# Performance work log

Hardware: AMD Instinct MI355X
Metric: run time of the kernel (lower is better)

The kernel has to match this reference:

```python
import jax, jax.numpy as jnp
import numpy as np

M, K, E = 4096, 7168, 2048  # tokens, hidden_size, expert_dim

def setup_inputs() -> dict:
    key = jax.random.key(0)
    k1, k2, k3 = jax.random.split(key, 3)
    x = jax.random.normal(k1, (M, K), dtype=jnp.float32)
    # NT layout: weights stored [n, k]
    w_up_gate = jax.random.normal(k2, (2 * E, K), dtype=jnp.float32) * (1.0 / np.sqrt(K))
    w_down = jax.random.normal(k3, (K, E), dtype=jnp.float32) * (1.0 / np.sqrt(E))
    return {"x": x, "w_up_gate": w_up_gate, "w_down": w_down}

def reference(x, w_up_gate, w_down):
    # up_gate GEMM: [m, k] @ [n, k]^T -> [m, 2*E]
    ug = jnp.einsum('mk,nk->mn', x, w_up_gate)
    gate, up = jnp.split(ug, 2, axis=-1)          # each [m, E]
    h = jax.nn.silu(gate) * up                     # SwiGLU activation
    # down GEMM: [m, E] @ [hidden, E]^T -> [m, hidden]
    out = jnp.einsum('me,he->mh', h, w_down)
    return out
```

## Files before the change

### kernel.cpp

```cpp
#include <hip/hip_runtime.h>
#include <hip/hip_bf16.h>
#include <stdint.h>

typedef __attribute__((ext_vector_type(8))) short     bf16x8;
typedef __attribute__((ext_vector_type(4))) float     f32x4;

__device__ __forceinline__ unsigned short f2bf(float f) {
  unsigned int u = __float_as_uint(f);
  u += 0x7FFFu + ((u >> 16) & 1u);
  return (unsigned short)(u >> 16);
}

__device__ __forceinline__ void async_cp16(const void* g, void* l) {
  __builtin_amdgcn_global_load_lds((const __attribute__((address_space(1))) void*)g,
                                   (__attribute__((address_space(3))) void*)l,
                                   16, 0, 0);
}

__global__ __launch_bounds__(256) void cvt_f32_to_bf16(const float* __restrict__ in,
                                                       unsigned short* __restrict__ out,
                                                       int n4) {
  int i = blockIdx.x * blockDim.x + threadIdx.x;
  const int stride = gridDim.x * blockDim.x;
  for (; i < n4; i += stride) {
    const float4 v = ((const float4*)in)[i];
    ushort4 o;
    o.x = f2bf(v.x); o.y = f2bf(v.y); o.z = f2bf(v.z); o.w = f2bf(v.w);
    ((ushort4*)out)[i] = o;
  }
}

__global__ __launch_bounds__(256) void cvt_wug_perm(const float* __restrict__ in,
                                                    unsigned short* __restrict__ out,
                                                    int n4) {
  int i = blockIdx.x * blockDim.x + threadIdx.x;
  const int stride = gridDim.x * blockDim.x;
  for (; i < n4; i += stride) {
    const int r = i / 1792, c = i - r * 1792;
    const int g = r >> 5, w = r & 31;
    const int src = g * 16 + (w & 15) + ((w & 16) ? 2048 : 0);
    const float4 v = ((const float4*)in)[(size_t)src * 1792 + c];
    ushort4 o;
    o.x = f2bf(v.x); o.y = f2bf(v.y); o.z = f2bf(v.z); o.w = f2bf(v.w);
    ((ushort4*)out)[(size_t)r * 1792 + c] = o;
  }
}

template <int K, int N, bool FUSE_SWIGLU>
__global__ __launch_bounds__(512, 2) void gemm_nt(const unsigned short* __restrict__ A,
                                                  const unsigned short* __restrict__ B,
                                                  void* __restrict__ Cv) {
  extern __shared__ char sm[];
  constexpr int nbx = N / 256;
  constexpr int nwg = (4096 / 256) * nbx;
  constexpr size_t K2 = (size_t)K * 2;

  const int bid = blockIdx.x;
  constexpr int q8 = nwg / 8;
  const int swz = (bid & 7) * q8 + (bid >> 3);
  const int bx = swz % nbx, by = swz / nbx;
  const int row0 = by * 256, col0 = bx * 256;

  const int tid = threadIdx.x, wave = tid >> 6, lane = tid & 63;
  const int wr = wave >> 2, wc = wave & 3;
  const int fr = lane & 15, fg = lane >> 4;

  const int l3 = lane >> 3;
  const int q  = (lane & 7) ^ l3;
  const int qr = q >> 2;
  const int qc = (q & 3) * 16;
  const char* gA[2]; const char* gB[2];
#pragma unroll
  for (int i = 0; i < 2; ++i) {
    const int L = i * 64 + wave * 8 + l3;
    gA[i] = (const char*)A + (size_t)(row0 + 2 * L + qr) * K2 + qc;
    gB[i] = (const char*)B + (size_t)(col0 + 2 * L + qr) * K2 + qc;
  }

  const int rbA = wr * 128 + fr;
  const int offA0 = (rbA >> 1) * 128 + (((((rbA & 1) << 2) | fg) ^ ((rbA >> 1) & 7)) << 4);
  const int rbB = wc * 64 + fr;
  const int offB0 = (rbB >> 1) * 128 + (((((rbB & 1) << 2) | fg) ^ ((rbB >> 1) & 7)) << 4);

  f32x4 acc[8][4];
#pragma unroll
  for (int m = 0; m < 8; ++m)
#pragma unroll
    for (int n = 0; n < 4; ++n) acc[m][n] = (f32x4){0.f, 0.f, 0.f, 0.f};

  constexpr int nh = K / 32;

#define STAGE_A(h, slot) do {                                   \
    char* d_ = sm + (slot) * 16384 + wave * 1024;               \
    async_cp16(gA[0] + (size_t)(h) * 64, d_);                   \
    async_cp16(gA[1] + (size_t)(h) * 64, d_ + 8192);            \
  } while (0)
#define STAGE_B(h, slot) do {                                   \
    char* d_ = sm + 65536 + (slot) * 16384 + wave * 1024;       \
    async_cp16(gB[0] + (size_t)(h) * 64, d_);                   \
    async_cp16(gB[1] + (size_t)(h) * 64, d_ + 8192);            \
  } while (0)

#pragma unroll
  for (int hp = 0; hp < 3; ++hp) { STAGE_A(hp, hp); STAGE_B(hp, hp); }
  asm volatile("s_waitcnt vmcnt(8)" ::: "memory");
  __builtin_amdgcn_s_barrier();

  for (int h = 0; h < nh; ++h) {
    const int slot = h & 3;
    const char* aBase = sm + slot * 16384;
    const char* bBase = sm + 65536 + slot * 16384;
    const int hs = (h + 3 < nh) ? h + 3 : nh - 1;
    const int sslot = (h + 3) & 3;

    bf16x8 af[4], bfr[4];
#pragma unroll
    for (int n = 0; n < 4; ++n) bfr[n] = *(const bf16x8*)(bBase + offB0 + n * 1024);
#pragma unroll
    for (int m = 0; m < 4; ++m) af[m] = *(const bf16x8*)(aBase + offA0 + m * 1024);
    STAGE_A(hs, sslot);
    __builtin_amdgcn_s_setprio(1);
#pragma unroll
    for (int m = 0; m < 4; ++m)
#pragma unroll
      for (int n = 0; n < 4; ++n)
        acc[m][n] = __builtin_amdgcn_mfma_f32_16x16x32_bf16(af[m], bfr[n], acc[m][n], 0, 0, 0);
    __builtin_amdgcn_s_setprio(0);

#pragma unroll
    for (int m = 0; m < 4; ++m) af[m] = *(const bf16x8*)(aBase + offA0 + (m + 4) * 1024);
    STAGE_B(hs, sslot);
    __builtin_amdgcn_s_setprio(1);
#pragma unroll
    for (int m = 0; m < 4; ++m)
#pragma unroll
      for (int n = 0; n < 4; ++n)
        acc[m + 4][n] = __builtin_amdgcn_mfma_f32_16x16x32_bf16(af[m], bfr[n], acc[m + 4][n], 0, 0, 0);
    __builtin_amdgcn_s_setprio(0);

    asm volatile("s_waitcnt vmcnt(8)" ::: "memory");
    __builtin_amdgcn_s_barrier();
  }
#undef STAGE_A
#undef STAGE_B

  const int rowb = row0 + wr * 128 + fg * 4;
  if (FUSE_SWIGLU) {
    unsigned short* Hp = (unsigned short*)Cv;
    const int ecb = ((col0 + wc * 64) >> 1) + fr;
#pragma unroll
    for (int m = 0; m < 8; ++m)
#pragma unroll
      for (int p = 0; p < 2; ++p)
#pragma unroll
        for (int j = 0; j < 4; ++j) {
          const float gv = acc[m][2 * p][j];
          const float uv = acc[m][2 * p + 1][j];
          const float s  = gv / (1.0f + __expf(-gv));
          Hp[(size_t)(rowb + m * 16 + j) * (N / 2) + (ecb + p * 16)] = f2bf(s * uv);
        }
  } else {
    float* Cp = (float*)Cv;
    const int colb = col0 + wc * 64 + fr;
#pragma unroll
    for (int m = 0; m < 8; ++m)
#pragma unroll
      for (int n = 0; n < 4; ++n)
#pragma unroll
        for (int j = 0; j < 4; ++j)
          Cp[(size_t)(rowb + m * 16 + j) * N + (colb + n * 16)] = acc[m][n][j];
  }
}

extern "C" void kernel_launch(void* const* d_in, const int* in_sizes, int n_in,
                              void* d_out, int out_size, void* d_ws, size_t ws_size,
                              hipStream_t stream) {
  const int M = 4096, K = 7168, E = 2048;

  const float* x   = (const float*)d_in[0];
  const float* wug = (const float*)d_in[1];
  const float* wd  = (const float*)d_in[2];
  float* out = (float*)d_out;

  char* ws = (char*)d_ws;
  unsigned short* xb  = (unsigned short*)(ws);
  unsigned short* wub = (unsigned short*)(ws + 58720256);
  unsigned short* wdb = (unsigned short*)(ws + 117440512);
  unsigned short* h   = (unsigned short*)(ws + 146800640);
  if (ws_size < 163577856) return;

  hipFuncSetAttribute((const void*)gemm_nt<7168, 4096, true>,
                      hipFuncAttributeMaxDynamicSharedMemorySize, 131072);
  hipFuncSetAttribute((const void*)gemm_nt<2048, 7168, false>,
                      hipFuncAttributeMaxDynamicSharedMemorySize, 131072);

  cvt_f32_to_bf16<<<2048, 256, 0, stream>>>(x,   xb,  M * K / 4);
  cvt_wug_perm  <<<2048, 256, 0, stream>>>(wug, wub, 2 * E * K / 4);
  cvt_f32_to_bf16<<<1024, 256, 0, stream>>>(wd,  wdb, K * E / 4);

  gemm_nt<7168, 4096, true><<<256, 512, 131072, stream>>>(xb, wub, h);

  gemm_nt<2048, 7168, false><<<448, 512, 131072, stream>>>(h, wdb, out);
}
```

Measured before the change: 388.9 us.

## Shrink GEMM tile to 256x128 with 4 waves and 3-stage LDS ring

Changes both GEMM kernels from 512-thread blocks computing 256x256 tiles to 256-thread blocks computing 256x128 tiles. This doubles the grid size and frees LDS so more blocks can be resident per CU. The prefetch pipeline drops from 4 slots to 3 at 24 KB each, and the A and B loads are merged into a single staging macro issued once per iteration. The goal is better occupancy and less wave-level tail imbalance, but each block now reuses less data, so more A traffic is loaded per unit of compute.

```diff
diff --git a/kernel.cpp b/kernel.cpp
--- a/kernel.cpp
+++ b/kernel.cpp
@@ -47,11 +47,11 @@
 }
 
 template <int K, int N, bool FUSE_SWIGLU>
-__global__ __launch_bounds__(512, 2) void gemm_nt(const unsigned short* __restrict__ A,
+__global__ __launch_bounds__(256, 2) void gemm_nt(const unsigned short* __restrict__ A,
                                                   const unsigned short* __restrict__ B,
                                                   void* __restrict__ Cv) {
   extern __shared__ char sm[];
-  constexpr int nbx = N / 256;
+  constexpr int nbx = N / 128;
   constexpr int nwg = (4096 / 256) * nbx;
   constexpr size_t K2 = (size_t)K * 2;
 
@@ -59,21 +59,25 @@
   constexpr int q8 = nwg / 8;
   const int swz = (bid & 7) * q8 + (bid >> 3);
   const int bx = swz % nbx, by = swz / nbx;
-  const int row0 = by * 256, col0 = bx * 256;
+  const int row0 = by * 256, col0 = bx * 128;
 
   const int tid = threadIdx.x, wave = tid >> 6, lane = tid & 63;
-  const int wr = wave >> 2, wc = wave & 3;
+  const int wr = wave >> 1, wc = wave & 1;
   const int fr = lane & 15, fg = lane >> 4;
 
   const int l3 = lane >> 3;
   const int q  = (lane & 7) ^ l3;
   const int qr = q >> 2;
   const int qc = (q & 3) * 16;
-  const char* gA[2]; const char* gB[2];
+  const char* gA[4]; const char* gB[2];
+#pragma unroll
+  for (int i = 0; i < 4; ++i) {
+    const int L = wave * 32 + i * 8 + l3;
+    gA[i] = (const char*)A + (size_t)(row0 + 2 * L + qr) * K2 + qc;
+  }
 #pragma unroll
   for (int i = 0; i < 2; ++i) {
-    const int L = i * 64 + wave * 8 + l3;
-    gA[i] = (const char*)A + (size_t)(row0 + 2 * L + qr) * K2 + qc;
+    const int L = wave * 16 + i * 8 + l3;
     gB[i] = (const char*)B + (size_t)(col0 + 2 * L + qr) * K2 + qc;
   }
 
@@ -90,35 +94,35 @@
 
   constexpr int nh = K / 32;
 
-#define STAGE_A(h, slot) do {                                   \
-    char* d_ = sm + (slot) * 16384 + wave * 1024;               \
-    async_cp16(gA[0] + (size_t)(h) * 64, d_);                   \
-    async_cp16(gA[1] + (size_t)(h) * 64, d_ + 8192);            \
+#define STAGE(hh, slot) do {                                        \
+    char* da = sm + (slot) * 24576 + wave * 4096;                   \
+    char* db = sm + (slot) * 24576 + 16384 + wave * 2048;           \
+    async_cp16(gA[0] + (size_t)(hh) * 64, da);                      \
+    async_cp16(gA[1] + (size_t)(hh) * 64, da + 1024);               \
+    async_cp16(gA[2] + (size_t)(hh) * 64, da + 2048);               \
+    async_cp16(gA[3] + (size_t)(hh) * 64, da + 3072);               \
+    async_cp16(gB[0] + (size_t)(hh) * 64, db);                      \
+    async_cp16(gB[1] + (size_t)(hh) * 64, db + 1024);               \
   } while (0)
-#define STAGE_B(h, slot) do {                                   \
-    char* d_ = sm + 65536 + (slot) * 16384 + wave * 1024;       \
-    async_cp16(gB[0] + (size_t)(h) * 64, d_);                   \
-    async_cp16(gB[1] + (size_t)(h) * 64, d_ + 8192);            \
-  } while (0)
-
-#pragma unroll
-  for (int hp = 0; hp < 3; ++hp) { STAGE_A(hp, hp); STAGE_B(hp, hp); }
-  asm volatile("s_waitcnt vmcnt(8)" ::: "memory");
+
+  STAGE(0, 0);
+  STAGE(1, 1);
+  asm volatile("s_waitcnt vmcnt(6)" ::: "memory");
   __builtin_amdgcn_s_barrier();
 
   for (int h = 0; h < nh; ++h) {
-    const int slot = h & 3;
-    const char* aBase = sm + slot * 16384;
-    const char* bBase = sm + 65536 + slot * 16384;
-    const int hs = (h + 3 < nh) ? h + 3 : nh - 1;
-    const int sslot = (h + 3) & 3;
+    const int slot  = h % 3;
+    const char* aBase = sm + slot * 24576;
+    const char* bBase = sm + slot * 24576 + 16384;
+    const int hs    = (h + 2 < nh) ? h + 2 : nh - 1;
+    const int sslot = (h + 2) % 3;
 
     bf16x8 af[4], bfr[4];
 #pragma unroll
     for (int n = 0; n < 4; ++n) bfr[n] = *(const bf16x8*)(bBase + offB0 + n * 1024);
 #pragma unroll
     for (int m = 0; m < 4; ++m) af[m] = *(const bf16x8*)(aBase + offA0 + m * 1024);
-    STAGE_A(hs, sslot);
+    STAGE(hs, sslot);
     __builtin_amdgcn_s_setprio(1);
 #pragma unroll
     for (int m = 0; m < 4; ++m)
@@ -129,7 +133,6 @@
 
 #pragma unroll
     for (int m = 0; m < 4; ++m) af[m] = *(const bf16x8*)(aBase + offA0 + (m + 4) * 1024);
-    STAGE_B(hs, sslot);
     __builtin_amdgcn_s_setprio(1);
 #pragma unroll
     for (int m = 0; m < 4; ++m)
@@ -138,11 +141,10 @@
         acc[m + 4][n] = __builtin_amdgcn_mfma_f32_16x16x32_bf16(af[m], bfr[n], acc[m + 4][n], 0, 0, 0);
     __builtin_amdgcn_s_setprio(0);
 
-    asm volatile("s_waitcnt vmcnt(8)" ::: "memory");
+    asm volatile("s_waitcnt vmcnt(6)" ::: "memory");
     __builtin_amdgcn_s_barrier();
   }
-#undef STAGE_A
-#undef STAGE_B
+#undef STAGE
 
   const int rowb = row0 + wr * 128 + fg * 4;
   if (FUSE_SWIGLU) {
@@ -190,15 +192,15 @@
   if (ws_size < 163577856) return;
 
   hipFuncSetAttribute((const void*)gemm_nt<7168, 4096, true>,
-                      hipFuncAttributeMaxDynamicSharedMemorySize, 131072);
+                      hipFuncAttributeMaxDynamicSharedMemorySize, 73728);
   hipFuncSetAttribute((const void*)gemm_nt<2048, 7168, false>,
-                      hipFuncAttributeMaxDynamicSharedMemorySize, 131072);
+                      hipFuncAttributeMaxDynamicSharedMemorySize, 73728);
 
   cvt_f32_to_bf16<<<2048, 256, 0, stream>>>(x,   xb,  M * K / 4);
   cvt_wug_perm  <<<2048, 256, 0, stream>>>(wug, wub, 2 * E * K / 4);
   cvt_f32_to_bf16<<<1024, 256, 0, stream>>>(wd,  wdb, K * E / 4);
 
-  gemm_nt<7168, 4096, true><<<256, 512, 131072, stream>>>(xb, wub, h);
-
-  gemm_nt<2048, 7168, false><<<448, 512, 131072, stream>>>(h, wdb, out);
-}
+  gemm_nt<7168, 4096, true><<<512, 256, 73728, stream>>>(xb, wub, h);
+
+  gemm_nt<2048, 7168, false><<<896, 256, 73728, stream>>>(h, wdb, out);
+}
```

After: 448.2 us. 1.15x slower.

## Restructure GEMM main loop into double-buffered 64-wide K tiles with quadrant phases

Applied to the files above, without the earlier changes.

Replaces the 4-slot, 32-wide K ring buffer with a two-buffer scheme that stages 64 K elements per tile. Each tile's compute is split into four MFMA quadrants separated by barriers, with A and B staging for the next tile interleaved between them. The aim is to halve loop-iteration overhead and cut per-k LDS fragment reloads by reusing fragments across quadrants. The cost is a shallower prefetch depth (one tile ahead, with a full vmcnt(0) wait each iteration), more barriers per tile, and more fragment registers.

```diff
diff --git a/kernel.cpp b/kernel.cpp
--- a/kernel.cpp
+++ b/kernel.cpp
@@ -54,6 +54,7 @@
   constexpr int nbx = N / 256;
   constexpr int nwg = (4096 / 256) * nbx;
   constexpr size_t K2 = (size_t)K * 2;
+  constexpr int nt = K / 64;
 
   const int bid = blockIdx.x;
   constexpr int q8 = nwg / 8;
@@ -65,16 +66,21 @@
   const int wr = wave >> 2, wc = wave & 3;
   const int fr = lane & 15, fg = lane >> 4;
 
-  const int l3 = lane >> 3;
-  const int q  = (lane & 7) ^ l3;
-  const int qr = q >> 2;
-  const int qc = (q & 3) * 16;
-  const char* gA[2]; const char* gB[2];
-#pragma unroll
-  for (int i = 0; i < 2; ++i) {
-    const int L = i * 64 + wave * 8 + l3;
-    gA[i] = (const char*)A + (size_t)(row0 + 2 * L + qr) * K2 + qc;
-    gB[i] = (const char*)B + (size_t)(col0 + 2 * L + qr) * K2 + qc;
+  const int pp = lane & 7, l3 = lane >> 3;
+  const char* srcA[4]; const char* srcB[4]; int dstA[4]; int dstB[4];
+#pragma unroll
+  for (int i = 0; i < 4; ++i) {
+    const int j  = wave * 4 + i;
+    const int kg = j >> 4;
+    const int lb = j & 15;
+    const int L  = lb * 8 + l3;
+    const int q  = pp ^ (L & 7);
+    const int qr = q >> 2;
+    const int qc = (q & 3) * 16;
+    srcA[i] = (const char*)A + (size_t)(row0 + 2 * L + qr) * K2 + kg * 64 + qc;
+    srcB[i] = (const char*)B + (size_t)(col0 + 2 * L + qr) * K2 + kg * 64 + qc;
+    dstA[i] = kg * 16384 + lb * 1024 + lane * 16;
+    dstB[i] = 32768 + dstA[i];
   }
 
   const int rbA = wr * 128 + fr;
@@ -88,57 +94,95 @@
 #pragma unroll
     for (int n = 0; n < 4; ++n) acc[m][n] = (f32x4){0.f, 0.f, 0.f, 0.f};
 
-  constexpr int nh = K / 32;
-
-#define STAGE_A(h, slot) do {                                   \
-    char* d_ = sm + (slot) * 16384 + wave * 1024;               \
-    async_cp16(gA[0] + (size_t)(h) * 64, d_);                   \
-    async_cp16(gA[1] + (size_t)(h) * 64, d_ + 8192);            \
+#define STAGE_A(tt, bufb) do {                                              \
+    _Pragma("unroll")                                                       \
+    for (int i_ = 0; i_ < 4; ++i_)                                          \
+      async_cp16(srcA[i_] + (size_t)(tt) * 128, (bufb) + dstA[i_]);         \
   } while (0)
-#define STAGE_B(h, slot) do {                                   \
-    char* d_ = sm + 65536 + (slot) * 16384 + wave * 1024;       \
-    async_cp16(gB[0] + (size_t)(h) * 64, d_);                   \
-    async_cp16(gB[1] + (size_t)(h) * 64, d_ + 8192);            \
+#define STAGE_B(tt, bufb) do {                                              \
+    _Pragma("unroll")                                                       \
+    for (int i_ = 0; i_ < 4; ++i_)                                          \
+      async_cp16(srcB[i_] + (size_t)(tt) * 128, (bufb) + dstB[i_]);         \
   } while (0)
 
-#pragma unroll
-  for (int hp = 0; hp < 3; ++hp) { STAGE_A(hp, hp); STAGE_B(hp, hp); }
-  asm volatile("s_waitcnt vmcnt(8)" ::: "memory");
+  STAGE_A(0, sm); STAGE_B(0, sm);
+  asm volatile("s_waitcnt vmcnt(0)" ::: "memory");
   __builtin_amdgcn_s_barrier();
 
-  for (int h = 0; h < nh; ++h) {
-    const int slot = h & 3;
-    const char* aBase = sm + slot * 16384;
-    const char* bBase = sm + 65536 + slot * 16384;
-    const int hs = (h + 3 < nh) ? h + 3 : nh - 1;
-    const int sslot = (h + 3) & 3;
-
-    bf16x8 af[4], bfr[4];
-#pragma unroll
-    for (int n = 0; n < 4; ++n) bfr[n] = *(const bf16x8*)(bBase + offB0 + n * 1024);
-#pragma unroll
-    for (int m = 0; m < 4; ++m) af[m] = *(const bf16x8*)(aBase + offA0 + m * 1024);
-    STAGE_A(hs, sslot);
-    __builtin_amdgcn_s_setprio(1);
-#pragma unroll
-    for (int m = 0; m < 4; ++m)
-#pragma unroll
-      for (int n = 0; n < 4; ++n)
-        acc[m][n] = __builtin_amdgcn_mfma_f32_16x16x32_bf16(af[m], bfr[n], acc[m][n], 0, 0, 0);
-    __builtin_amdgcn_s_setprio(0);
-
-#pragma unroll
-    for (int m = 0; m < 4; ++m) af[m] = *(const bf16x8*)(aBase + offA0 + (m + 4) * 1024);
-    STAGE_B(hs, sslot);
-    __builtin_amdgcn_s_setprio(1);
-#pragma unroll
-    for (int m = 0; m < 4; ++m)
-#pragma unroll
-      for (int n = 0; n < 4; ++n)
-        acc[m + 4][n] = __builtin_amdgcn_mfma_f32_16x16x32_bf16(af[m], bfr[n], acc[m + 4][n], 0, 0, 0);
-    __builtin_amdgcn_s_setprio(0);
-
-    asm volatile("s_waitcnt vmcnt(8)" ::: "memory");
+  bf16x8 af[2][4], bfA[2][2], bfB[2][2];
+
+  for (int t = 0; t < nt; ++t) {
+    char* cur = sm + (t & 1) * 65536;
+    char* nxt = sm + ((t + 1) & 1) * 65536;
+    const bool do_stage = (t + 1 < nt);
+
+#pragma unroll
+    for (int kg = 0; kg < 2; ++kg) {
+#pragma unroll
+      for (int mt = 0; mt < 4; ++mt)
+        af[kg][mt] = *(const bf16x8*)(cur + kg * 16384 + offA0 + mt * 1024);
+#pragma unroll
+      for (int nn = 0; nn < 2; ++nn)
+        bfA[kg][nn] = *(const bf16x8*)(cur + 32768 + kg * 16384 + offB0 + nn * 1024);
+    }
+    if (do_stage) STAGE_A(t + 1, nxt);
+    __builtin_amdgcn_s_barrier();
+    __builtin_amdgcn_s_setprio(1);
+#pragma unroll
+    for (int mt = 0; mt < 4; ++mt)
+#pragma unroll
+      for (int nn = 0; nn < 2; ++nn)
+#pragma unroll
+        for (int kg = 0; kg < 2; ++kg)
+          acc[mt][nn] = __builtin_amdgcn_mfma_f32_16x16x32_bf16(af[kg][mt], bfA[kg][nn], acc[mt][nn], 0, 0, 0);
+    __builtin_amdgcn_s_setprio(0);
+    __builtin_amdgcn_s_barrier();
+
+#pragma unroll
+    for (int kg = 0; kg < 2; ++kg)
+#pragma unroll
+      for (int nn = 0; nn < 2; ++nn)
+        bfB[kg][nn] = *(const bf16x8*)(cur + 32768 + kg * 16384 + offB0 + (2 + nn) * 1024);
+    if (do_stage) STAGE_B(t + 1, nxt);
+    __builtin_amdgcn_s_barrier();
+    __builtin_amdgcn_s_setprio(1);
+#pragma unroll
+    for (int mt = 0; mt < 4; ++mt)
+#pragma unroll
+      for (int nn = 0; nn < 2; ++nn)
+#pragma unroll
+        for (int kg = 0; kg < 2; ++kg)
+          acc[mt][2 + nn] = __builtin_amdgcn_mfma_f32_16x16x32_bf16(af[kg][mt], bfB[kg][nn], acc[mt][2 + nn], 0, 0, 0);
+    __builtin_amdgcn_s_setprio(0);
+    __builtin_amdgcn_s_barrier();
+
+#pragma unroll
+    for (int kg = 0; kg < 2; ++kg)
+#pragma unroll
+      for (int mt = 0; mt < 4; ++mt)
+        af[kg][mt] = *(const bf16x8*)(cur + kg * 16384 + offA0 + (4 + mt) * 1024);
+    __builtin_amdgcn_s_barrier();
+    __builtin_amdgcn_s_setprio(1);
+#pragma unroll
+    for (int mt = 0; mt < 4; ++mt)
+#pragma unroll
+      for (int nn = 0; nn < 2; ++nn)
+#pragma unroll
+        for (int kg = 0; kg < 2; ++kg)
+          acc[4 + mt][2 + nn] = __builtin_amdgcn_mfma_f32_16x16x32_bf16(af[kg][mt], bfB[kg][nn], acc[4 + mt][2 + nn], 0, 0, 0);
+    __builtin_amdgcn_s_setprio(0);
+    __builtin_amdgcn_s_barrier();
+
+    __builtin_amdgcn_s_setprio(1);
+#pragma unroll
+    for (int mt = 0; mt < 4; ++mt)
+#pragma unroll
+      for (int nn = 0; nn < 2; ++nn)
+#pragma unroll
+        for (int kg = 0; kg < 2; ++kg)
+          acc[4 + mt][nn] = __builtin_amdgcn_mfma_f32_16x16x32_bf16(af[kg][mt], bfA[kg][nn], acc[4 + mt][nn], 0, 0, 0);
+    __builtin_amdgcn_s_setprio(0);
+    asm volatile("s_waitcnt vmcnt(0)" ::: "memory");
     __builtin_amdgcn_s_barrier();
   }
 #undef STAGE_A
```

Result: slower. 424.9 us (+9.2%).

## Switch GEMMs to 32x32x16 MFMA with 4-wave blocks and 3-stage pipeline

Applied to the files above, without the earlier changes.

Replaces the 16x16x32 bf16 MFMA tiles with 32x32x16 MFMA, giving each wave a 128x128 output tile and shrinking the workgroup from 8 waves to 4 with launch bounds of 1 block. The LDS pipeline drops from 4 stages to 3 (96KB). The gate/up weight permutation interleave widens to 32 rows to match the new accumulator layout. The aim is fewer LDS reads per FLOP and denser MFMA issue, at the cost of higher register pressure and fewer waves to hide latency.

```diff
diff --git a/kernel.cpp b/kernel.cpp
--- a/kernel.cpp
+++ b/kernel.cpp
@@ -2,8 +2,8 @@
 #include <hip/hip_bf16.h>
 #include <stdint.h>
 
-typedef __attribute__((ext_vector_type(8))) short     bf16x8;
-typedef __attribute__((ext_vector_type(4))) float     f32x4;
+typedef __attribute__((ext_vector_type(8)))  short bf16x8;
+typedef __attribute__((ext_vector_type(16))) float f32x16;
 
 __device__ __forceinline__ unsigned short f2bf(float f) {
   unsigned int u = __float_as_uint(f);
@@ -37,8 +37,8 @@
   const int stride = gridDim.x * blockDim.x;
   for (; i < n4; i += stride) {
     const int r = i / 1792, c = i - r * 1792;
-    const int g = r >> 5, w = r & 31;
-    const int src = g * 16 + (w & 15) + ((w & 16) ? 2048 : 0);
+    const int g = r >> 6, w = r & 63;
+    const int src = g * 32 + (w & 31) + ((w & 32) ? 2048 : 0);
     const float4 v = ((const float4*)in)[(size_t)src * 1792 + c];
     ushort4 o;
     o.x = f2bf(v.x); o.y = f2bf(v.y); o.z = f2bf(v.z); o.w = f2bf(v.w);
@@ -47,13 +47,14 @@
 }
 
 template <int K, int N, bool FUSE_SWIGLU>
-__global__ __launch_bounds__(512, 2) void gemm_nt(const unsigned short* __restrict__ A,
+__global__ __launch_bounds__(256, 1) void gemm_nt(const unsigned short* __restrict__ A,
                                                   const unsigned short* __restrict__ B,
                                                   void* __restrict__ Cv) {
   extern __shared__ char sm[];
   constexpr int nbx = N / 256;
   constexpr int nwg = (4096 / 256) * nbx;
   constexpr size_t K2 = (size_t)K * 2;
+  constexpr int nh = K / 32;
 
   const int bid = blockIdx.x;
   constexpr int q8 = nwg / 8;
@@ -62,80 +63,104 @@
   const int row0 = by * 256, col0 = bx * 256;
 
   const int tid = threadIdx.x, wave = tid >> 6, lane = tid & 63;
-  const int wr = wave >> 2, wc = wave & 3;
-  const int fr = lane & 15, fg = lane >> 4;
-
-  const int l3 = lane >> 3;
-  const int q  = (lane & 7) ^ l3;
-  const int qr = q >> 2;
-  const int qc = (q & 3) * 16;
-  const char* gA[2]; const char* gB[2];
-#pragma unroll
-  for (int i = 0; i < 2; ++i) {
-    const int L = i * 64 + wave * 8 + l3;
-    gA[i] = (const char*)A + (size_t)(row0 + 2 * L + qr) * K2 + qc;
-    gB[i] = (const char*)B + (size_t)(col0 + 2 * L + qr) * K2 + qc;
-  }
-
-  const int rbA = wr * 128 + fr;
-  const int offA0 = (rbA >> 1) * 128 + (((((rbA & 1) << 2) | fg) ^ ((rbA >> 1) & 7)) << 4);
-  const int rbB = wc * 64 + fr;
-  const int offB0 = (rbB >> 1) * 128 + (((((rbB & 1) << 2) | fg) ^ ((rbB >> 1) & 7)) << 4);
-
-  f32x4 acc[8][4];
-#pragma unroll
-  for (int m = 0; m < 8; ++m)
-#pragma unroll
-    for (int n = 0; n < 4; ++n) acc[m][n] = (f32x4){0.f, 0.f, 0.f, 0.f};
-
-  constexpr int nh = K / 32;
-
-#define STAGE_A(h, slot) do {                                   \
-    char* d_ = sm + (slot) * 16384 + wave * 1024;               \
-    async_cp16(gA[0] + (size_t)(h) * 64, d_);                   \
-    async_cp16(gA[1] + (size_t)(h) * 64, d_ + 8192);            \
+  const int wr = wave >> 1, wc = wave & 1;
+  const int l31 = lane & 31, hi = lane >> 5;
+
+  const int p7 = lane & 7, l3 = lane >> 3;
+  const int qs  = p7 ^ l3;
+  const int qr  = qs >> 2;
+  const int qc  = (qs & 3) * 16;
+  int offsA[4], offsB[4], dstOff[4];
+#pragma unroll
+  for (int i = 0; i < 4; ++i) {
+    const int j = wave * 4 + i;
+    const int L = j * 8 + l3;
+    offsA[i] = (row0 + 2 * L + qr) * (int)K2 + qc;
+    offsB[i] = (col0 + 2 * L + qr) * (int)K2 + qc;
+    dstOff[i] = j * 1024 + lane * 16;
+  }
+  const char* Ab = (const char*)A;
+  const char* Bb = (const char*)B;
+
+  const int lin = l31 >> 1;
+  const int qb  = (lane & 1) * 4 + hi;
+  const int l7  = lin & 7;
+  const int offA[2] = { (wr * 64 + lin) * 128 + ((qb    ) ^ l7) * 16,
+                        (wr * 64 + lin) * 128 + ((qb + 2) ^ l7) * 16 };
+  const int offB[2] = { (wc * 64 + lin) * 128 + ((qb    ) ^ l7) * 16,
+                        (wc * 64 + lin) * 128 + ((qb + 2) ^ l7) * 16 };
+
+  f32x16 acc[4][4];
+#pragma unroll
+  for (int m = 0; m < 4; ++m)
+#pragma unroll
+    for (int n = 0; n < 4; ++n)
+#pragma unroll
+      for (int j = 0; j < 16; ++j) acc[m][n][j] = 0.f;
+
+#define STAGE_A(hh, slot) do {                                              \
+    _Pragma("unroll")                                                       \
+    for (int i_ = 0; i_ < 4; ++i_)                                          \
+      async_cp16(Ab + offsA[i_] + (size_t)(hh) * 64,                        \
+                 sm + (slot) * 32768 + dstOff[i_]);                         \
   } while (0)
-#define STAGE_B(h, slot) do {                                   \
-    char* d_ = sm + 65536 + (slot) * 16384 + wave * 1024;       \
-    async_cp16(gB[0] + (size_t)(h) * 64, d_);                   \
-    async_cp16(gB[1] + (size_t)(h) * 64, d_ + 8192);            \
+#define STAGE_B(hh, slot) do {                                              \
+    _Pragma("unroll")                                                       \
+    for (int i_ = 0; i_ < 4; ++i_)                                          \
+      async_cp16(Bb + offsB[i_] + (size_t)(hh) * 64,                        \
+                 sm + (slot) * 32768 + 16384 + dstOff[i_]);                 \
   } while (0)
 
-#pragma unroll
-  for (int hp = 0; hp < 3; ++hp) { STAGE_A(hp, hp); STAGE_B(hp, hp); }
+  STAGE_A(0, 0); STAGE_B(0, 0);
+  STAGE_A(1, 1); STAGE_B(1, 1);
   asm volatile("s_waitcnt vmcnt(8)" ::: "memory");
   __builtin_amdgcn_s_barrier();
 
   for (int h = 0; h < nh; ++h) {
-    const int slot = h & 3;
-    const char* aBase = sm + slot * 16384;
-    const char* bBase = sm + 65536 + slot * 16384;
-    const int hs = (h + 3 < nh) ? h + 3 : nh - 1;
-    const int sslot = (h + 3) & 3;
-
-    bf16x8 af[4], bfr[4];
-#pragma unroll
-    for (int n = 0; n < 4; ++n) bfr[n] = *(const bf16x8*)(bBase + offB0 + n * 1024);
-#pragma unroll
-    for (int m = 0; m < 4; ++m) af[m] = *(const bf16x8*)(aBase + offA0 + m * 1024);
-    STAGE_A(hs, sslot);
+    const int slot = h % 3;
+    const char* aBase = sm + slot * 32768;
+    const char* bBase = aBase + 16384;
+    const int hs = (h + 2 < nh) ? h + 2 : nh - 1;
+    const int ss = (h + 2) % 3;
+
+    bf16x8 bfr[4][2], af[2][2];
+#pragma unroll
+    for (int nt = 0; nt < 4; ++nt)
+#pragma unroll
+      for (int kh = 0; kh < 2; ++kh)
+        bfr[nt][kh] = *(const bf16x8*)(bBase + nt * 2048 + offB[kh]);
+#pragma unroll
+    for (int mt = 0; mt < 2; ++mt)
+#pragma unroll
+      for (int kh = 0; kh < 2; ++kh)
+        af[mt][kh] = *(const bf16x8*)(aBase + mt * 2048 + offA[kh]);
+    STAGE_A(hs, ss);
+
     __builtin_amdgcn_s_setprio(1);
 #pragma unroll
-    for (int m = 0; m < 4; ++m)
-#pragma unroll
-      for (int n = 0; n < 4; ++n)
-        acc[m][n] = __builtin_amdgcn_mfma_f32_16x16x32_bf16(af[m], bfr[n], acc[m][n], 0, 0, 0);
+    for (int kh = 0; kh < 2; ++kh)
+#pragma unroll
+      for (int mt = 0; mt < 2; ++mt)
+#pragma unroll
+        for (int nt = 0; nt < 4; ++nt)
+          acc[mt][nt] = __builtin_amdgcn_mfma_f32_32x32x16_bf16(af[mt][kh], bfr[nt][kh], acc[mt][nt], 0, 0, 0);
     __builtin_amdgcn_s_setprio(0);
 
 #pragma unroll
-    for (int m = 0; m < 4; ++m) af[m] = *(const bf16x8*)(aBase + offA0 + (m + 4) * 1024);
-    STAGE_B(hs, sslot);
+    for (int mt = 0; mt < 2; ++mt)
+#pragma unroll
+      for (int kh = 0; kh < 2; ++kh)
+        af[mt][kh] = *(const bf16x8*)(aBase + (mt + 2) * 2048 + offA[kh]);
+    STAGE_B(hs, ss);
+
     __builtin_amdgcn_s_setprio(1);
 #pragma unroll
-    for (int m = 0; m < 4; ++m)
-#pragma unroll
-      for (int n = 0; n < 4; ++n)
-        acc[m + 4][n] = __builtin_amdgcn_mfma_f32_16x16x32_bf16(af[m], bfr[n], acc[m + 4][n], 0, 0, 0);
+    for (int kh = 0; kh < 2; ++kh)
+#pragma unroll
+      for (int mt = 0; mt < 2; ++mt)
+#pragma unroll
+        for (int nt = 0; nt < 4; ++nt)
+          acc[mt + 2][nt] = __builtin_amdgcn_mfma_f32_32x32x16_bf16(af[mt][kh], bfr[nt][kh], acc[mt + 2][nt], 0, 0, 0);
     __builtin_amdgcn_s_setprio(0);
 
     asm volatile("s_waitcnt vmcnt(8)" ::: "memory");
@@ -144,31 +169,34 @@
 #undef STAGE_A
 #undef STAGE_B
 
-  const int rowb = row0 + wr * 128 + fg * 4;
+  const int rowb = row0 + wr * 128;
   if (FUSE_SWIGLU) {
     unsigned short* Hp = (unsigned short*)Cv;
-    const int ecb = ((col0 + wc * 64) >> 1) + fr;
-#pragma unroll
-    for (int m = 0; m < 8; ++m)
-#pragma unroll
-      for (int p = 0; p < 2; ++p)
-#pragma unroll
-        for (int j = 0; j < 4; ++j) {
-          const float gv = acc[m][2 * p][j];
-          const float uv = acc[m][2 * p + 1][j];
+    const int ecb = ((col0 + wc * 128) >> 1) + l31;
+#pragma unroll
+    for (int mt = 0; mt < 4; ++mt)
+#pragma unroll
+      for (int t = 0; t < 2; ++t)
+#pragma unroll
+        for (int j = 0; j < 16; ++j) {
+          const int row = rowb + mt * 32 + (j & 3) + 8 * (j >> 2) + 4 * hi;
+          const float gv = acc[mt][2 * t][j];
+          const float uv = acc[mt][2 * t + 1][j];
           const float s  = gv / (1.0f + __expf(-gv));
-          Hp[(size_t)(rowb + m * 16 + j) * (N / 2) + (ecb + p * 16)] = f2bf(s * uv);
+          Hp[(size_t)row * (N / 2) + (ecb + t * 32)] = f2bf(s * uv);
         }
   } else {
     float* Cp = (float*)Cv;
-    const int colb = col0 + wc * 64 + fr;
-#pragma unroll
-    for (int m = 0; m < 8; ++m)
-#pragma unroll
-      for (int n = 0; n < 4; ++n)
-#pragma unroll
-        for (int j = 0; j < 4; ++j)
-          Cp[(size_t)(rowb + m * 16 + j) * N + (colb + n * 16)] = acc[m][n][j];
+    const int colb = col0 + wc * 128 + l31;
+#pragma unroll
+    for (int mt = 0; mt < 4; ++mt)
+#pragma unroll
+      for (int nt = 0; nt < 4; ++nt)
+#pragma unroll
+        for (int j = 0; j < 16; ++j) {
+          const int row = rowb + mt * 32 + (j & 3) + 8 * (j >> 2) + 4 * hi;
+          Cp[(size_t)row * N + (colb + nt * 32)] = acc[mt][nt][j];
+        }
   }
 }
 
@@ -190,15 +218,15 @@
   if (ws_size < 163577856) return;
 
   hipFuncSetAttribute((const void*)gemm_nt<7168, 4096, true>,
-                      hipFuncAttributeMaxDynamicSharedMemorySize, 131072);
+                      hipFuncAttributeMaxDynamicSharedMemorySize, 98304);
   hipFuncSetAttribute((const void*)gemm_nt<2048, 7168, false>,
-                      hipFuncAttributeMaxDynamicSharedMemorySize, 131072);
+                      hipFuncAttributeMaxDynamicSharedMemorySize, 98304);
 
   cvt_f32_to_bf16<<<2048, 256, 0, stream>>>(x,   xb,  M * K / 4);
   cvt_wug_perm  <<<2048, 256, 0, stream>>>(wug, wub, 2 * E * K / 4);
   cvt_f32_to_bf16<<<1024, 256, 0, stream>>>(wd,  wdb, K * E / 4);
 
-  gemm_nt<7168, 4096, true><<<256, 512, 131072, stream>>>(xb, wub, h);
-
-  gemm_nt<2048, 7168, false><<<448, 512, 131072, stream>>>(h, wdb, out);
-}
+  gemm_nt<7168, 4096, true><<<256, 256, 98304, stream>>>(xb, wub, h);
+
+  gemm_nt<2048, 7168, false><<<448, 256, 98304, stream>>>(h, wdb, out);
+}
```

Measured after the change: 479.1 us. 1.23x slower.
